# Optimization experiments

Hardware: AMD Instinct MI355X
Metric: run time of the kernel (lower is better)

The kernel has to match this reference:

```python
import jax, jax.numpy as jnp
import numpy as np
import math

DIM = 2048
NUM_HEADS = 16
HEAD_DIM = DIM // NUM_HEADS
BATCH = 4
SEQ = 2048
ROPE_BASE = 10000.0


def setup_inputs() -> dict:
    key = jax.random.key(0)
    ks = jax.random.split(key, 6)
    s = 1.0 / math.sqrt(DIM)
    return {
        "x": jax.random.normal(ks[0], (BATCH, SEQ, DIM), dtype=jnp.float32),
        "Wq": jax.random.normal(ks[1], (DIM, DIM), dtype=jnp.float32) * s,
        "Wk": jax.random.normal(ks[2], (DIM, DIM), dtype=jnp.float32) * s,
        "Wv": jax.random.normal(ks[3], (DIM, DIM), dtype=jnp.float32) * s,
        "Wo": jax.random.normal(ks[4], (DIM, DIM), dtype=jnp.float32) * s,
        "bo": jnp.zeros((DIM,), dtype=jnp.float32),
    }


def _apply_rope(t, pos):
    # t: [B, H, S, D]; standard rotate-half RoPE per head
    d = t.shape[-1]
    inv_freq = 1.0 / (ROPE_BASE ** (jnp.arange(0, d, 2, dtype=jnp.float32) / d))  # [D/2]
    ang = pos.astype(jnp.float32)[:, None] * inv_freq[None, :]  # [S, D/2]
    cos = jnp.concatenate([jnp.cos(ang), jnp.cos(ang)], axis=-1)  # [S, D]
    sin = jnp.concatenate([jnp.sin(ang), jnp.sin(ang)], axis=-1)
    t1, t2 = t[..., : d // 2], t[..., d // 2:]
    rot = jnp.concatenate([-t2, t1], axis=-1)
    return t * cos + rot * sin


def reference(x, Wq, Wk, Wv, Wo, bo):
    B, S, D = x.shape
    H, Hd = NUM_HEADS, HEAD_DIM
    # projections (torch Linear: x @ W.T)
    q = (x @ Wq.T).reshape(B, S, H, Hd).transpose(0, 2, 1, 3)  # [B,H,S,Hd]
    k = (x @ Wk.T).reshape(B, S, H, Hd).transpose(0, 2, 1, 3)
    v = (x @ Wv.T).reshape(B, S, H, Hd).transpose(0, 2, 1, 3)
    pos = jnp.arange(S)
    q = _apply_rope(q, pos)
    k = _apply_rope(k, pos)
    scores = jnp.einsum("bhqd,bhkd->bhqk", q, k) / math.sqrt(Hd)
    causal = jnp.tril(jnp.ones((S, S), dtype=bool))
    scores = jnp.where(causal, scores, -1e9)
    w = jax.nn.softmax(scores, axis=-1)
    out = jnp.einsum("bhqk,bhkd->bhqd", w, v)  # [B,H,S,Hd]
    out = out.transpose(0, 2, 1, 3).reshape(B, S, D)
    return out @ Wo.T + bo
```

## Files before the change

kernel.cpp:

```cpp
#include <hip/hip_runtime.h>

#define BATCH 4
#define SEQ   2048
#define DIM   2048
#define NH    16
#define HD    128

typedef __bf16 bf16x8 __attribute__((ext_vector_type(8)));
typedef float  f32x4  __attribute__((ext_vector_type(4)));

__device__ __forceinline__ unsigned short f2bf(float f) {
  unsigned int u = __builtin_bit_cast(unsigned int, f);
  u += 0x7fffu + ((u >> 16) & 1u);
  return (unsigned short)(u >> 16);
}

__device__ __forceinline__ void async16(void* lds, const void* g) {
  __builtin_amdgcn_global_load_lds(
      (const __attribute__((address_space(1))) unsigned int*)g,
      (__attribute__((address_space(3))) unsigned int*)lds, 16, 0, 0);
}

__global__ __launch_bounds__(256) void cast_all_kernel(
    const float* __restrict__ x,
    const float* __restrict__ w0, const float* __restrict__ w1,
    const float* __restrict__ w2, const float* __restrict__ w3,
    unsigned short* __restrict__ dst) {
  int i = blockIdx.x * 256 + threadIdx.x;
  const float* s;
  int loc;
  if (i < (1 << 22)) { s = x; loc = i; }
  else {
    int k = i - (1 << 22);
    int sel = k >> 20; loc = k & 0xfffff;
    s = sel == 0 ? w0 : sel == 1 ? w1 : sel == 2 ? w2 : w3;
  }
  float4 v = ((const float4*)s)[loc];
  ushort4 o;
  o.x = f2bf(v.x); o.y = f2bf(v.y); o.z = f2bf(v.z); o.w = f2bf(v.w);
  ((ushort4*)dst)[i] = o;
}

__global__ __launch_bounds__(256) void gemm_qkv(
    const unsigned short* __restrict__ A,
    const unsigned short* __restrict__ Wq,
    const unsigned short* __restrict__ Wk,
    const unsigned short* __restrict__ Wv,
    unsigned short* __restrict__ Qo,
    unsigned short* __restrict__ Ko,
    unsigned short* __restrict__ Vto) {
  __shared__ unsigned short As[128 * 32];
  __shared__ unsigned short Bs[128 * 32];
  __shared__ float ep[32 * 132];
  const int tid = threadIdx.x;
  const int lane = tid & 63, wv = tid >> 6;
  const int q15 = lane & 15, quad = lane >> 4;
  const int wm = wv >> 1, wn = wv & 1;
  const int gx = blockIdx.x;
  const int sel = gx >> 4, h = gx & 15;
  const int m0 = blockIdx.y * 128;
  const unsigned short* Bw =
      (sel == 0 ? Wq : (sel == 1 ? Wk : Wv)) + (size_t)h * 128 * DIM;

  f32x4 acc[4][4] = {};

  for (int kt = 0; kt < DIM; kt += 32) {
    __syncthreads();
#pragma unroll
    for (int i = 0; i < 2; ++i) {
      int l = i * 256 + tid;
      int r = l >> 2, s = l & 3;
      int c = (s - (r >> 1)) & 3;
      async16(&As[l * 8], A + (size_t)(m0 + r) * DIM + kt + c * 8);
    }
#pragma unroll
    for (int i = 0; i < 2; ++i) {
      int l = i * 256 + tid;
      int r = l >> 2, s = l & 3;
      int c = (s - (r >> 1)) & 3;
      async16(&Bs[l * 8], Bw + (size_t)r * DIM + kt + c * 8);
    }
    __syncthreads();

    bf16x8 af[4], bf[4];
#pragma unroll
    for (int mf = 0; mf < 4; ++mf) {
      int r = wm * 64 + mf * 16 + q15;
      int sl = r * 4 + ((quad + (r >> 1)) & 3);
      af[mf] = *(const bf16x8*)&As[sl * 8];
    }
#pragma unroll
    for (int nf = 0; nf < 4; ++nf) {
      int r = wn * 64 + nf * 16 + q15;
      int sl = r * 4 + ((quad + (r >> 1)) & 3);
      bf[nf] = *(const bf16x8*)&Bs[sl * 8];
    }
#pragma unroll
    for (int mf = 0; mf < 4; ++mf)
#pragma unroll
      for (int nf = 0; nf < 4; ++nf)
        acc[mf][nf] = __builtin_amdgcn_mfma_f32_16x16x32_bf16(af[mf], bf[nf], acc[mf][nf], 0, 0, 0);
  }

  const int b = m0 >> 11;
  const int s0 = m0 & (SEQ - 1);
  const int bh = b * NH + h;
  const float CS = 0.12751744f;

  float invf[2][8];
  if (sel < 2) {
#pragma unroll
    for (int oi = 0; oi < 2; ++oi) {
      int oc = ((oi * 256 + tid) & 15) * 8;
#pragma unroll
      for (int j = 0; j < 8; ++j)
        invf[oi][j] = exp2f(-(float)((oc & 63) + j) * 0.20762050593046932f);
    }
  }

  for (int c = 0; c < 4; ++c) {
    __syncthreads();
    if (wm == (c >> 1)) {
      int mfb = (c & 1) * 2;
#pragma unroll
      for (int mi = 0; mi < 2; ++mi) {
        int mf = mfb + mi;
        int rr0 = mf * 16 + quad * 4 - (c & 1) * 32;
#pragma unroll
        for (int nf = 0; nf < 4; ++nf) {
          int col = wn * 64 + nf * 16 + q15;
#pragma unroll
          for (int r = 0; r < 4; ++r)
            ep[(rr0 + r) * 132 + col] = acc[mf][nf][r];
        }
      }
    }
    __syncthreads();
#pragma unroll
    for (int oi = 0; oi < 2; ++oi) {
      int o = oi * 256 + tid;
      if (sel < 2) {
        int rr = o >> 4, oc = (o & 15) * 8;
        int s = s0 + c * 32 + rr;
        float sf = (float)s;
        float4 a0 = *(const float4*)&ep[rr * 132 + oc];
        float4 a1 = *(const float4*)&ep[rr * 132 + oc + 4];
        float4 b0 = *(const float4*)&ep[rr * 132 + (oc ^ 64)];
        float4 b1 = *(const float4*)&ep[rr * 132 + (oc ^ 64) + 4];
        float av[8] = {a0.x, a0.y, a0.z, a0.w, a1.x, a1.y, a1.z, a1.w};
        float bv[8] = {b0.x, b0.y, b0.z, b0.w, b1.x, b1.y, b1.z, b1.w};
        float sgn = (oc & 64) ? 1.f : -1.f;
        float scl = (sel == 0) ? CS : 1.0f;
        unsigned short u[8];
#pragma unroll
        for (int j = 0; j < 8; ++j) {
          float ang = sf * invf[oi][j];
          float cc = __cosf(ang), ss = __sinf(ang);
          u[j] = f2bf((av[j] * cc + sgn * bv[j] * ss) * scl);
        }
        unsigned short* dst = (sel == 0 ? Qo : Ko) + ((size_t)bh * SEQ + s) * HD + oc;
        *(uint4*)dst = *(uint4*)u;
      } else {
        int hd = o & 127, so8 = (o >> 7) * 8;
        unsigned short u[8];
#pragma unroll
        for (int k = 0; k < 8; ++k)
          u[k] = f2bf(ep[(so8 + k) * 132 + hd]);
        *(uint4*)(Vto + ((size_t)bh * HD + hd) * SEQ + (s0 + c * 32 + so8)) = *(uint4*)u;
      }
    }
  }
}

#define STAGE8(buf, op, half, kt)                                               \
  do {                                                                          \
    const unsigned short* Gp = (op) ? Bw : A;                                   \
    const int rb = ((op) ? n0 : m0) + (half) * 128;                             \
    unsigned short* hb = sm + ((((buf) << 1) | (op)) * 2 + (half)) * 8192;      \
    _Pragma("unroll")                                                           \
    for (int jj = 0; jj < 2; ++jj) {                                            \
      int l = jj * 512 + tid;                                                   \
      int rr = l >> 3, cc = l & 7;                                              \
      int cs = cc ^ (rr & 7);                                                   \
      async16(&hb[l * 8], Gp + (size_t)(rb + rr) * DIM + (kt) * 64 + cs * 8);   \
    }                                                                           \
  } while (0)

#define RDA8(dst, buf, mf, ks)                                                  \
  do {                                                                          \
    int R = (mf) * 16 + q15;                                                    \
    int cc = ((ks) * 4 + quad) ^ (R & 7);                                       \
    dst = *(const bf16x8*)&sm[((((buf) << 1) | 0) * 2 + wm) * 8192 + (R * 8 + cc) * 8]; \
  } while (0)

#define RDB8(dst, buf, nf, ks)                                                  \
  do {                                                                          \
    int R = (wn & 1) * 64 + (nf) * 16 + q15;                                    \
    int cc = ((ks) * 4 + quad) ^ (R & 7);                                       \
    dst = *(const bf16x8*)&sm[((((buf) << 1) | 1) * 2 + (wn >> 1)) * 8192 + (R * 8 + cc) * 8]; \
  } while (0)

#define MFMA_Q(mlo, nlo)                                                        \
  do {                                                                          \
    __builtin_amdgcn_s_barrier();                                               \
    asm volatile("s_waitcnt lgkmcnt(0)" ::: "memory");                          \
    __builtin_amdgcn_s_setprio(1);                                              \
    _Pragma("unroll")                                                           \
    for (int ks = 0; ks < 2; ++ks)                                              \
      _Pragma("unroll")                                                         \
      for (int mi = 0; mi < 4; ++mi)                                            \
        _Pragma("unroll")                                                       \
        for (int ni = 0; ni < 2; ++ni)                                          \
          acc[(mlo) + mi][(nlo) + ni] = __builtin_amdgcn_mfma_f32_16x16x32_bf16( \
              af[(mlo) + mi][ks], bfr[(nlo) + ni][ks], acc[(mlo) + mi][(nlo) + ni], 0, 0, 0); \
    __builtin_amdgcn_s_setprio(0);                                              \
    __builtin_amdgcn_s_barrier();                                               \
  } while (0)

__global__ __launch_bounds__(512, 2) void gemm_out(
    const unsigned short* __restrict__ A,
    const unsigned short* __restrict__ Bw,
    float* __restrict__ outf,
    const float* __restrict__ bias) {
  extern __shared__ unsigned short sm[];
  const int tid = threadIdx.x;
  const int lane = tid & 63;
  const int wv = tid >> 6;
  const int q15 = lane & 15, quad = lane >> 4;
  const int wm = wv >> 2, wn = wv & 3;
  const int n0 = blockIdx.x * 256, m0 = blockIdx.y * 256;

  f32x4 acc[8][4] = {};
  bf16x8 af[8][2], bfr[4][2];

  STAGE8(0, 0, 0, 0); STAGE8(0, 0, 1, 0); STAGE8(0, 1, 0, 0); STAGE8(0, 1, 1, 0);
  STAGE8(1, 0, 0, 1); STAGE8(1, 0, 1, 1);
  asm volatile("s_waitcnt vmcnt(4)" ::: "memory");
  __builtin_amdgcn_s_barrier();

  for (int T = 0; T < 32; ++T) {
    const int buf = T & 1;
#pragma unroll
    for (int mf = 0; mf < 4; ++mf) { RDA8(af[mf][0], buf, mf, 0); RDA8(af[mf][1], buf, mf, 1); }
#pragma unroll
    for (int nf = 0; nf < 2; ++nf) { RDB8(bfr[nf][0], buf, nf, 0); RDB8(bfr[nf][1], buf, nf, 1); }
    if (T + 1 < 32) STAGE8(buf ^ 1, 1, 0, T + 1);
    MFMA_Q(0, 0);
#pragma unroll
    for (int mf = 4; mf < 8; ++mf) { RDA8(af[mf][0], buf, mf, 0); RDA8(af[mf][1], buf, mf, 1); }
#pragma unroll
    for (int nf = 2; nf < 4; ++nf) { RDB8(bfr[nf][0], buf, nf, 0); RDB8(bfr[nf][1], buf, nf, 1); }
    if (T + 1 < 32) STAGE8(buf ^ 1, 1, 1, T + 1);
    MFMA_Q(0, 2);
    if (T + 2 < 32) STAGE8(buf, 0, 0, T + 2);
    MFMA_Q(4, 2);
    if (T + 2 < 32) STAGE8(buf, 0, 1, T + 2);
    if (T < 30) { asm volatile("s_waitcnt vmcnt(4)" ::: "memory"); }
    else if (T == 30) { asm volatile("s_waitcnt vmcnt(0)" ::: "memory"); }
    MFMA_Q(4, 0);
  }

  float bv[4];
#pragma unroll
  for (int nf = 0; nf < 4; ++nf) bv[nf] = bias[n0 + wn * 64 + nf * 16 + q15];
#pragma unroll
  for (int mf = 0; mf < 8; ++mf)
#pragma unroll
    for (int nf = 0; nf < 4; ++nf) {
      int col = n0 + wn * 64 + nf * 16 + q15;
      int row = m0 + wm * 128 + mf * 16 + quad * 4;
#pragma unroll
      for (int r = 0; r < 4; ++r)
        outf[(size_t)(row + r) * DIM + col] = acc[mf][nf][r] + bv[nf];
    }
}

__global__ __launch_bounds__(256) void attn_kernel(
    const unsigned short* __restrict__ Q,
    const unsigned short* __restrict__ Kg,
    const unsigned short* __restrict__ Vt,
    unsigned short* __restrict__ O) {
  __shared__ unsigned short Ks[64 * 128];
  __shared__ unsigned short Vs[128 * 64];
  __shared__ unsigned short Ps[4 * 32 * 72];
  const int tid = threadIdx.x;
  const int lane = tid & 63, wv = tid >> 6;
  const int q15 = lane & 15, quad = lane >> 4;
  const int bh = blockIdx.x & 63;
  const int t = blockIdx.x >> 6;
  const int nseg = (t < 8) ? 1 : 2;
  const int b = bh >> 4, h = bh & 15;
  unsigned short* Pw = Ps + wv * (32 * 72);

  for (int seg = 0; seg < nseg; ++seg) {
    const int qt = (t < 8) ? (15 - t) : (seg == 0 ? (15 - t) : (t - 8));
    const int q0w = qt * 128 + wv * 32;

    bf16x8 qf[2][4];
#pragma unroll
    for (int nq = 0; nq < 2; ++nq) {
      const unsigned short* qp = Q + ((size_t)bh * SEQ + q0w + nq * 16 + q15) * HD + quad * 8;
#pragma unroll
      for (int ks = 0; ks < 4; ++ks) qf[nq][ks] = *(const bf16x8*)(qp + ks * 32);
    }

    f32x4 oacc[2][8] = {};
    float rs[2] = {0.f, 0.f};
    const int jmax = 2 * qt + 2;
    const int jcap = 2 * qt + (wv >> 1);

    for (int j = 0; j < jmax; ++j) {
      const int kv0 = j * 64;
      __syncthreads();
#pragma unroll
      for (int i = 0; i < 4; ++i) {
        int l = i * 256 + tid;
        int r = l >> 4, c = (l & 15) ^ (r & 15);
        async16(&Ks[l * 8], Kg + ((size_t)bh * SEQ + kv0 + r) * HD + c * 8);
      }
#pragma unroll
      for (int i = 0; i < 4; ++i) {
        int l = i * 256 + tid;
        int r = l >> 3, c = (l & 7) ^ (r & 7);
        async16(&Vs[l * 8], Vt + ((size_t)bh * HD + r) * SEQ + kv0 + c * 8);
      }
      __syncthreads();

      if (j <= jcap) {
        const bool edge = (j == jcap);
#pragma unroll
        for (int mi = 0; mi < 4; ++mi) {
          f32x4 st[2] = {};
#pragma unroll
          for (int ks = 0; ks < 4; ++ks) {
            int r = mi * 16 + q15;
            int c = ks * 4 + quad;
            bf16x8 kf = *(const bf16x8*)&Ks[(r * 16 + (c ^ (r & 15))) * 8];
#pragma unroll
            for (int nq = 0; nq < 2; ++nq)
              st[nq] = __builtin_amdgcn_mfma_f32_16x16x32_bf16(kf, qf[nq][ks], st[nq], 0, 0, 0);
          }
#pragma unroll
          for (int nq = 0; nq < 2; ++nq) {
            unsigned int u[4];
#pragma unroll
            for (int r = 0; r < 4; ++r) {
              float p = exp2f(st[nq][r]);
              if (edge) {
                int kv = kv0 + mi * 16 + quad * 4 + r;
                int qq = q0w + nq * 16 + q15;
                p = (kv > qq) ? 0.f : p;
              }
              unsigned int uu = __builtin_bit_cast(unsigned int, p) & 0xffff0000u;
              rs[nq] += __builtin_bit_cast(float, uu);
              u[r] = uu;
            }
            uint2 pk;
            pk.x = (u[0] >> 16) | u[1];
            pk.y = (u[2] >> 16) | u[3];
            *(uint2*)&Pw[(nq * 16 + q15) * 72 + mi * 16 + quad * 4] = pk;
          }
        }
#pragma unroll
        for (int ks = 0; ks < 2; ++ks) {
          bf16x8 pf[2];
#pragma unroll
          for (int mq = 0; mq < 2; ++mq)
            pf[mq] = *(const bf16x8*)&Pw[(mq * 16 + q15) * 72 + ks * 32 + quad * 8];
#pragma unroll
          for (int nf = 0; nf < 8; ++nf) {
            int r = nf * 16 + q15;
            int c = ks * 4 + quad;
            bf16x8 vf = *(const bf16x8*)&Vs[(r * 8 + (c ^ (r & 7))) * 8];
#pragma unroll
            for (int mq = 0; mq < 2; ++mq)
              oacc[mq][nf] = __builtin_amdgcn_mfma_f32_16x16x32_bf16(pf[mq], vf, oacc[mq][nf], 0, 0, 0);
          }
        }
      }
    }

#pragma unroll
    for (int nq = 0; nq < 2; ++nq) {
      rs[nq] += __shfl_xor(rs[nq], 16);
      rs[nq] += __shfl_xor(rs[nq], 32);
    }
#pragma unroll
    for (int mq = 0; mq < 2; ++mq) {
#pragma unroll
      for (int r = 0; r < 4; ++r) {
        float l = __shfl(rs[mq], quad * 4 + r);
        float inv = 1.0f / l;
        int qq = q0w + mq * 16 + quad * 4 + r;
        size_t base = (((size_t)b * SEQ + qq) * NH + h) * HD;
#pragma unroll
        for (int nf = 0; nf < 8; ++nf)
          O[base + nf * 16 + q15] = f2bf(oacc[mq][nf][r] * inv);
      }
    }
  }
}

extern "C" void kernel_launch(void* const* d_in, const int* in_sizes, int n_in,
                              void* d_out, int out_size, void* d_ws, size_t ws_size,
                              hipStream_t stream) {
  (void)in_sizes; (void)n_in; (void)out_size; (void)ws_size;
  const float* x  = (const float*)d_in[0];
  const float* Wq = (const float*)d_in[1];
  const float* Wk = (const float*)d_in[2];
  const float* Wv = (const float*)d_in[3];
  const float* Wo = (const float*)d_in[4];
  const float* bo = (const float*)d_in[5];
  float* out = (float*)d_out;

  const size_t XE = (size_t)BATCH * SEQ * DIM;
  const size_t WE = (size_t)DIM * DIM;

  char* p = (char*)d_ws;
  unsigned short* xb   = (unsigned short*)p; p += XE * 2;
  unsigned short* Wall = (unsigned short*)p; p += 4 * WE * 2;
  unsigned short* Qg   = (unsigned short*)p; p += XE * 2;
  unsigned short* Kb   = (unsigned short*)p; p += XE * 2;
  unsigned short* Vtb  = (unsigned short*)p; p += XE * 2;
  unsigned short* attn = (unsigned short*)p; p += XE * 2;

  static bool attr_set = false;
  if (!attr_set) {
    hipFuncSetAttribute((const void*)gemm_out,
                        hipFuncAttributeMaxDynamicSharedMemorySize, 131072);
    attr_set = true;
  }

  cast_all_kernel<<<(int)(2 * XE / 4 / 256), 256, 0, stream>>>(x, Wq, Wk, Wv, Wo, xb);

  gemm_qkv<<<dim3(48, 64), 256, 0, stream>>>(
      xb, Wall, Wall + WE, Wall + 2 * WE, Qg, Kb, Vtb);

  attn_kernel<<<dim3(768), 256, 0, stream>>>(Qg, Kb, Vtb, attn);

  gemm_out<<<dim3(DIM / 256, (BATCH * SEQ) / 256), 512, 131072, stream>>>(
      attn, Wall + 3 * WE, out, bo);
}
```

Before: 678.0 us.

## Double-buffer K tiles in attention and pair query tiles per block

```diff
diff --git a/kernel.cpp b/kernel.cpp
--- a/kernel.cpp
+++ b/kernel.cpp
@@ -280,20 +280,19 @@
     const unsigned short* __restrict__ Kg,
     const unsigned short* __restrict__ Vt,
     unsigned short* __restrict__ O) {
-  __shared__ unsigned short Ks[64 * 128];
+  __shared__ unsigned short Ks[2][64 * 128];
   __shared__ unsigned short Vs[128 * 64];
   __shared__ unsigned short Ps[4 * 32 * 72];
   const int tid = threadIdx.x;
   const int lane = tid & 63, wv = tid >> 6;
   const int q15 = lane & 15, quad = lane >> 4;
   const int bh = blockIdx.x & 63;
-  const int t = blockIdx.x >> 6;
-  const int nseg = (t < 8) ? 1 : 2;
+  const int slot = blockIdx.x >> 6;
   const int b = bh >> 4, h = bh & 15;
   unsigned short* Pw = Ps + wv * (32 * 72);
 
-  for (int seg = 0; seg < nseg; ++seg) {
-    const int qt = (t < 8) ? (15 - t) : (seg == 0 ? (15 - t) : (t - 8));
+  for (int seg = 0; seg < 2; ++seg) {
+    const int qt = (seg == 0) ? (15 - slot) : slot;
     const int q0w = qt * 128 + wv * 32;
 
     bf16x8 qf[2][4];
@@ -309,25 +308,37 @@
     const int jmax = 2 * qt + 2;
     const int jcap = 2 * qt + (wv >> 1);
 
+#pragma unroll
+    for (int i = 0; i < 4; ++i) {
+      int l = i * 256 + tid;
+      int r = l >> 4, c = (l & 15) ^ (r & 15);
+      async16(&Ks[0][l * 8], Kg + ((size_t)bh * SEQ + r) * HD + c * 8);
+    }
+#pragma unroll
+    for (int i = 0; i < 4; ++i) {
+      int l = i * 256 + tid;
+      int r = l >> 3, c = (l & 7) ^ (r & 7);
+      async16(&Vs[l * 8], Vt + ((size_t)bh * HD + r) * SEQ + c * 8);
+    }
+    asm volatile("s_waitcnt vmcnt(0)" ::: "memory");
+    __builtin_amdgcn_s_barrier();
+
     for (int j = 0; j < jmax; ++j) {
       const int kv0 = j * 64;
-      __syncthreads();
-#pragma unroll
-      for (int i = 0; i < 4; ++i) {
-        int l = i * 256 + tid;
-        int r = l >> 4, c = (l & 15) ^ (r & 15);
-        async16(&Ks[l * 8], Kg + ((size_t)bh * SEQ + kv0 + r) * HD + c * 8);
-      }
-#pragma unroll
-      for (int i = 0; i < 4; ++i) {
-        int l = i * 256 + tid;
-        int r = l >> 3, c = (l & 7) ^ (r & 7);
-        async16(&Vs[l * 8], Vt + ((size_t)bh * HD + r) * SEQ + kv0 + c * 8);
-      }
-      __syncthreads();
+      if (j + 1 < jmax) {
+        unsigned short* kb = Ks[(j + 1) & 1];
+        const int kn = kv0 + 64;
+#pragma unroll
+        for (int i = 0; i < 4; ++i) {
+          int l = i * 256 + tid;
+          int r = l >> 4, c = (l & 15) ^ (r & 15);
+          async16(&kb[l * 8], Kg + ((size_t)bh * SEQ + kn + r) * HD + c * 8);
+        }
+      }
 
       if (j <= jcap) {
         const bool edge = (j == jcap);
+        const unsigned short* kb = Ks[j & 1];
 #pragma unroll
         for (int mi = 0; mi < 4; ++mi) {
           f32x4 st[2] = {};
@@ -335,7 +346,7 @@
           for (int ks = 0; ks < 4; ++ks) {
             int r = mi * 16 + q15;
             int c = ks * 4 + quad;
-            bf16x8 kf = *(const bf16x8*)&Ks[(r * 16 + (c ^ (r & 15))) * 8];
+            bf16x8 kf = *(const bf16x8*)&kb[(r * 16 + (c ^ (r & 15))) * 8];
 #pragma unroll
             for (int nq = 0; nq < 2; ++nq)
               st[nq] = __builtin_amdgcn_mfma_f32_16x16x32_bf16(kf, qf[nq][ks], st[nq], 0, 0, 0);
@@ -361,6 +372,13 @@
             *(uint2*)&Pw[(nq * 16 + q15) * 72 + mi * 16 + quad * 4] = pk;
           }
         }
+      }
+
+      if (j + 1 < jmax) { asm volatile("s_waitcnt vmcnt(4)" ::: "memory"); }
+      else              { asm volatile("s_waitcnt vmcnt(0)" ::: "memory"); }
+      __builtin_amdgcn_s_barrier();
+
+      if (j <= jcap) {
 #pragma unroll
         for (int ks = 0; ks < 2; ++ks) {
           bf16x8 pf[2];
@@ -377,6 +395,20 @@
               oacc[mq][nf] = __builtin_amdgcn_mfma_f32_16x16x32_bf16(pf[mq], vf, oacc[mq][nf], 0, 0, 0);
           }
         }
+      }
+
+      __builtin_amdgcn_s_barrier();
+
+      if (j + 1 < jmax) {
+        const int kn = kv0 + 64;
+#pragma unroll
+        for (int i = 0; i < 4; ++i) {
+          int l = i * 256 + tid;
+          int r = l >> 3, c = (l & 7) ^ (r & 7);
+          async16(&Vs[l * 8], Vt + ((size_t)bh * HD + r) * SEQ + kn + c * 8);
+        }
+        asm volatile("s_waitcnt vmcnt(4)" ::: "memory");
+        __builtin_amdgcn_s_barrier();
       }
     }
 
@@ -436,7 +468,7 @@
   gemm_qkv<<<dim3(48, 64), 256, 0, stream>>>(
       xb, Wall, Wall + WE, Wall + 2 * WE, Qg, Kb, Vtb);
 
-  attn_kernel<<<dim3(768), 256, 0, stream>>>(Qg, Kb, Vtb, attn);
+  attn_kernel<<<dim3(512), 256, 0, stream>>>(Qg, Kb, Vtb, attn);
 
   gemm_out<<<dim3(DIM / 256, (BATCH * SEQ) / 256), 512, 131072, stream>>>(
       attn, Wall + 3 * WE, out, bo);
```

After: 718.4 us. +5.9%, slower.
